# Kernel optimization log

Hardware: AMD Instinct MI355X
Metric: run time of the kernel (lower is better)

## Reference

```python
import jax, jax.numpy as jnp
import numpy as np

BUF = 16  # max polygon vertex buffer (convex 9-gon clipped by 4 half-planes -> <= 13 verts)


def _shoelace(V, c):
    # area of polygon stored in buffer V[:c]
    i = jnp.arange(V.shape[0])
    nxt = jnp.where(i + 1 < c, i + 1, 0)
    Vn = V[nxt]
    contrib = jnp.where(i < c, V[:, 0] * Vn[:, 1] - Vn[:, 0] * V[:, 1], 0.0)
    return 0.5 * jnp.abs(contrib.sum())


def _convex_hull(P):
    # exact convex hull of n small points; returns CCW-ordered vertex buffer [BUF,2] and count
    n = P.shape[0]
    d = P[None, :, :] - P[:, None, :]  # p_j - p_i
    minc = jnp.full((n, n), jnp.inf, P.dtype)
    for k in range(n):  # fixed small loop, keeps memory at [n,n]
        w = (P[k] - P)[:, None, :]
        minc = jnp.minimum(minc, d[..., 0] * w[..., 1] - d[..., 1] * w[..., 0])
    minc = jax.lax.stop_gradient(minc)  # hull membership is discrete
    edge = (minc >= -1e-6) & (~jnp.eye(n, dtype=bool))  # (i,j) is CCW hull edge iff all pts left
    hull = edge.any(1)
    cnt = hull.sum()
    cen = (P * hull[:, None]).sum(0) / jnp.maximum(cnt, 1)
    ang = jnp.arctan2(P[:, 1] - cen[1], P[:, 0] - cen[0])
    keyv = jnp.where(hull, jax.lax.stop_gradient(ang), jnp.inf)
    order = jnp.argsort(keyv)
    V = jnp.zeros((BUF, 2), P.dtype).at[:n].set(P[order])
    return V, cnt


def _clip(V, c, a, b):
    # Sutherland-Hodgman clip of convex polygon (V,c) by half-plane left of a->b
    i = jnp.arange(BUF)
    active = i < c
    nxt = jnp.where(i + 1 < c, i + 1, 0)
    nx = V[nxt]
    e = b - a
    s_cur = e[0] * (V[:, 1] - a[1]) - e[1] * (V[:, 0] - a[0])
    s_nxt = e[0] * (nx[:, 1] - a[1]) - e[1] * (nx[:, 0] - a[0])
    in_cur = s_cur >= 0
    in_nxt = s_nxt >= 0
    den = s_cur - s_nxt
    safe = jnp.abs(den) > 1e-9
    t = jnp.where(safe, s_cur / jnp.where(safe, den, 1.0), 0.0)
    ipt = V + t[:, None] * (nx - V)
    f_int = active & (in_cur != in_nxt)
    f_nxt = active & in_nxt
    pts = jnp.stack([ipt, nx], 1).reshape(2 * BUF, 2)
    flg = jnp.stack([f_int, f_nxt], 1).reshape(2 * BUF)
    pos = jnp.cumsum(flg) - 1
    idx = jnp.where(flg, pos, BUF)  # invalid slots dropped
    out = jnp.zeros((BUF, 2), V.dtype).at[idx].set(pts, mode='drop')
    return out, flg.sum()


def _order_ccw(Q):
    cen = Q.mean(0)
    ang = jnp.arctan2(Q[:, 1] - cen[1], Q[:, 0] - cen[0])
    return Q[jnp.argsort(jax.lax.stop_gradient(ang))]


def _per_point(gt4, p9):
    # giou_loss + out_of_box loss for one (gt quad, 9 pred points) pair
    gt = _order_ccw(gt4)
    Vp, cp = _convex_hull(p9)          # predicted convex polygon (OrientedRepPoints convex hull)
    a_pred = _shoelace(Vp, cp)
    a_gt = _shoelace(jnp.zeros((BUF, 2), gt.dtype).at[:4].set(gt), 4)
    V, c = Vp, cp
    for e in range(4):
        V, c = _clip(V, c, gt[e], gt[(e + 1) % 4])
    a_int = _shoelace(V, c)
    union = a_pred + a_gt - a_int
    iou = a_int / (union + 1e-16)
    Vh, ch = _convex_hull(jnp.concatenate([gt4, p9], 0))  # hull of all 13 points
    a_hull = _shoelace(Vh, ch)
    giou = iou - (a_hull - union) / (a_hull + 1e-16)
    # out-of-box distance: positive distance of pred points outside the gt quad edges
    b = jnp.roll(gt, -1, 0)
    e2 = b - gt
    rel = p9[:, None, :] - gt[None, :, :]
    s = (e2[None, :, 0] * rel[..., 1] - e2[None, :, 1] * rel[..., 0]) / (jnp.linalg.norm(e2, axis=1)[None, :] + 1e-9)
    oob = jax.nn.relu((-s).max(1)).mean()
    return 1.0 - giou, oob


def _assign(points_xy, points_lvl, gt_obb):
    # OBBPointAssigner: sequential per-GT closest-point assignment (pos_num=1, scale=4)
    xs = gt_obb[:, 0::2]
    ys = gt_obb[:, 1::2]
    xmin, xmax = xs.min(1), xs.max(1)
    ymin, ymax = ys.min(1), ys.max(1)
    cxy = jnp.stack([(xmin + xmax) / 2, (ymin + ymax) / 2], 1)
    wh = jnp.maximum(jnp.stack([xmax - xmin, ymax - ymin], 1), 1e-6)
    lvl_min, lvl_max = points_lvl.min(), points_lvl.max()
    glvl = jnp.clip(((jnp.log2(wh[:, 0] / 4.0) + jnp.log2(wh[:, 1] / 4.0)) / 2).astype(jnp.int32), lvl_min, lvl_max)
    K = gt_obb.shape[0]
    Np = points_xy.shape[0]

    def body(carry, g):
        inds, dist = carry
        c_xy, c_wh, c_lvl, gi = g
        dmask = points_lvl == c_lvl
        dd = jnp.linalg.norm((points_xy - c_xy) / c_wh, axis=1)
        dd = jnp.where(dmask, dd, jnp.inf)
        j = jnp.argmin(dd)
        md = dd[j]
        better = md < dist[j]
        inds = inds.at[j].set(jnp.where(better, gi + 1, inds[j]))
        dist = dist.at[j].set(jnp.where(better, md, dist[j]))
        return (inds, dist), None

    init = (jnp.zeros(Np, jnp.int32), jnp.full(Np, jnp.inf, points_xy.dtype))
    (inds, _), _ = jax.lax.scan(body, init, (cxy, wh, glvl, jnp.arange(K, dtype=jnp.int32)))
    return inds


def _stage(rep, inds, labels, gt_obb):
    posm = (labels > 0).astype(rep.dtype)
    gidx = jnp.maximum(inds - 1, 0)
    gt4 = gt_obb[gidx].reshape(-1, 4, 2)
    p9 = rep.reshape(-1, 9, 2)
    gl, oob = jax.vmap(_per_point)(gt4, p9)
    npos = jnp.maximum(posm.sum(), 1.0)
    return (gl * posm).sum() / npos, (oob * posm).sum() / npos


def _forward(rpi, rpr, cls, stride, gob, glab):
    stride = jax.lax.stop_gradient(stride)
    plvl = jnp.log2(stride).astype(jnp.int32)
    inds_i = _assign(jax.lax.stop_gradient(rpi[:, 8:10]), plvl, jax.lax.stop_gradient(gob))
    inds_r = _assign(jax.lax.stop_gradient(rpr[:, 8:10]), plvl, jax.lax.stop_gradient(gob))
    lab_i = jnp.where(inds_i > 0, glab[jnp.maximum(inds_i - 1, 0)], 0)
    lab_r = jnp.where(inds_r > 0, glab[jnp.maximum(inds_r - 1, 0)], 0)
    loc_i, sc_i = _stage(rpi, inds_i, lab_i, gob)
    loc_r, sc_r = _stage(rpr, inds_r, lab_r, gob)
    logp = jax.nn.log_softmax(cls, -1)
    cls_loss = -jnp.take_along_axis(logp, lab_r[:, None], 1).mean()
    return 1.0 * cls_loss + 0.3 * loc_i + 1.0 * loc_r + 0.05 * sc_i + 0.1 * sc_r


def setup_inputs() -> dict:
    key = jax.random.key(0)
    ks = jax.random.split(key, 8)
    strides = [8, 16, 32, 64, 128]
    batch = 2
    centers_list, stride_list = [], []
    for s in strides:
        hw = 1536 // s
        c = (jnp.arange(hw, dtype=jnp.float32) + 0.5) * s
        gx, gy = jnp.meshgrid(c, c, indexing='ij')
        cen = jnp.stack([gx.reshape(-1), gy.reshape(-1)], 1)
        cen = jnp.tile(cen, (batch, 1))
        centers_list.append(cen)
        stride_list.append(jnp.full((cen.shape[0],), float(s), jnp.float32))
    centers = jnp.concatenate(centers_list, 0)
    points_stride = jnp.concatenate(stride_list, 0)
    N = centers.shape[0]  # 98208
    base = jnp.tile(centers[:, None, :], (1, 9, 1)).reshape(N, 18)
    scale18 = jnp.repeat(points_stride[:, None], 18, 1)
    rpi = base + jax.random.normal(ks[0], (N, 18), jnp.float32) * scale18 * 1.5
    rpr = base + jax.random.normal(ks[1], (N, 18), jnp.float32) * scale18 * 1.0
    classification = jax.random.normal(ks[2], (N, 16), jnp.float32)
    K = 64
    cx = jax.random.uniform(ks[3], (K,), minval=128.0, maxval=1408.0)
    cy = jax.random.uniform(ks[4], (K,), minval=128.0, maxval=1408.0)
    w = jax.random.uniform(ks[5], (K,), minval=48.0, maxval=400.0)
    h = jax.random.uniform(ks[6], (K,), minval=48.0, maxval=400.0)
    th = jax.random.uniform(ks[7], (K,), minval=0.0, maxval=float(np.pi))
    ct, st = jnp.cos(th), jnp.sin(th)
    dx = jnp.stack([-w, w, w, -w], 1) / 2
    dy = jnp.stack([-h, -h, h, h], 1) / 2
    xs = cx[:, None] + dx * ct[:, None] - dy * st[:, None]
    ys = cy[:, None] + dx * st[:, None] + dy * ct[:, None]
    gt_obboxes = jnp.stack([xs, ys], 2).reshape(K, 8)
    gt_labels = jax.random.randint(jax.random.fold_in(key, 7), (K,), 1, 16)
    return {"rep_points_init": rpi, "rep_points_refine": rpr, "classification": classification,
            "points_stride": points_stride, "gt_obboxes": gt_obboxes, "gt_labels": gt_labels}


def reference(rep_points_init, rep_points_refine, classification, points_stride, gt_obboxes, gt_labels):
    return _forward(rep_points_init, rep_points_refine, classification, points_stride, gt_obboxes, gt_labels)
```

## Files before the change

kernel.cpp:

```cpp
#include <hip/hip_runtime.h>
#include <math.h>
#include <stdint.h>

#pragma clang fp contract(off)

#define SUB 16

struct WS {
  double sums[8];
  unsigned long long packed[128];
  int lo[8], hi[8];
  float gcx[64], gcy[64], gw[64], gh[64];
  int glvl[64];
  unsigned cntpub[2];
  unsigned done2;
  unsigned pad0;
  double clsPart[1024];
};

__global__ void __launch_bounds__(256) k_pre(const float* __restrict__ rpi,
                                             const float* __restrict__ rpr,
                                             const float* __restrict__ cls,
                                             const float* __restrict__ stridev,
                                             const float* __restrict__ gob,
                                             int N, int K, WS* ws) {
  __shared__ double sd[256];
  __shared__ int bnd[9];
  __shared__ int slmin, slmax;
  int t = threadIdx.x;
  float2* xyi = (float2*)(ws + 1);
  float2* xyr = xyi + N;

  if (blockIdx.x == 0) {
    if (t < 8) ws->sums[t] = 0.0;
    if (t < 128) ws->packed[t] = ~0ULL;
    if (t == 0) { ws->done2 = 0u; ws->cntpub[0] = 0u; ws->cntpub[1] = 0u; }
    if (t < 9) {
      float v = (float)(1 << t);
      int lo = 0, hi = N;
      while (lo < hi) { int mid = (lo + hi) >> 1; if (stridev[mid] < v) lo = mid + 1; else hi = mid; }
      bnd[t] = lo;
    }
    __syncthreads();
    if (t == 0) {
      int a = 7, b = 0;
      for (int l = 0; l < 8; l++) {
        int lo2 = bnd[l], hi2 = bnd[l + 1];
        ws->lo[l] = lo2; ws->hi[l] = hi2;
        if (hi2 > lo2) { if (l < a) a = l; if (l > b) b = l; }
      }
      slmin = a; slmax = b;
    }
    __syncthreads();
    if (t < K && t < 64) {
      const float* g = gob + t * 8;
      float x0 = g[0], x1 = g[2], x2 = g[4], x3 = g[6];
      float y0 = g[1], y1 = g[3], y2 = g[5], y3 = g[7];
      float xmin = fminf(fminf(x0, x1), fminf(x2, x3));
      float xmax = fmaxf(fmaxf(x0, x1), fmaxf(x2, x3));
      float ymin = fminf(fminf(y0, y1), fminf(y2, y3));
      float ymax = fmaxf(fmaxf(y0, y1), fmaxf(y2, y3));
      float w = fmaxf(xmax - xmin, 1e-6f);
      float h = fmaxf(ymax - ymin, 1e-6f);
      ws->gcx[t] = (xmin + xmax) * 0.5f;
      ws->gcy[t] = (ymin + ymax) * 0.5f;
      ws->gw[t] = w; ws->gh[t] = h;
      int gl = (int)((log2f(w * 0.25f) + log2f(h * 0.25f)) * 0.5f);
      gl = gl < slmin ? slmin : (gl > slmax ? slmax : gl);
      ws->glvl[t] = gl;
    }
  }

  double acc = 0.0;
  for (int i = blockIdx.x * 256 + t; i < N; i += gridDim.x * 256) {
    const float* pi = rpi + (size_t)i * 18;
    const float* pr = rpr + (size_t)i * 18;
    xyi[i] = *(const float2*)(pi + 8);
    xyr[i] = *(const float2*)(pr + 8);
    const float4* r = (const float4*)(cls + (size_t)i * 16);
    float4 q0 = r[0], q1 = r[1], q2 = r[2], q3 = r[3];
    float x[16] = {q0.x, q0.y, q0.z, q0.w, q1.x, q1.y, q1.z, q1.w,
                   q2.x, q2.y, q2.z, q2.w, q3.x, q3.y, q3.z, q3.w};
    float m = x[0];
    for (int j = 1; j < 16; j++) m = fmaxf(m, x[j]);
    float ssum = 0.f;
    for (int j = 0; j < 16; j++) ssum += expf(x[j] - m);
    acc += (double)(logf(ssum) + m - x[0]);
  }
  sd[t] = acc;
  __syncthreads();
  for (int off = 128; off > 0; off >>= 1) {
    if (t < off) sd[t] += sd[t + off];
    __syncthreads();
  }
  if (t == 0) ws->clsPart[blockIdx.x] = sd[0];
}

__global__ void __launch_bounds__(256) k_main(int N, int K, WS* ws) {
  __shared__ unsigned long long sb[256];
  int t = threadIdx.x;
  int b = blockIdx.x;
  int s = b % SUB;
  int ak = b / SUB;
  int a = ak / K;
  int k = ak % K;
  int L = ws->glvl[k];
  int lo = ws->lo[L], hi = ws->hi[L];
  float cx = ws->gcx[k], cy = ws->gcy[k], w = ws->gw[k], h = ws->gh[k];
  const float2* xy = (const float2*)(ws + 1) + (a ? N : 0);
  unsigned long long best = ~0ULL;
  for (int i = lo + s * 256 + t; i < hi; i += SUB * 256) {
    float2 p = xy[i];
    float dx = (p.x - cx) / w, dy = (p.y - cy) / h;
    float dd = sqrtf(dx * dx + dy * dy);
    unsigned long long pk = ((unsigned long long)__float_as_uint(dd) << 32) | (unsigned)i;
    if (pk < best) best = pk;
  }
  sb[t] = best;
  __syncthreads();
  for (int off = 128; off > 0; off >>= 1) {
    if (t < off) { unsigned long long o = sb[t + off]; if (o < sb[t]) sb[t] = o; }
    __syncthreads();
  }
  if (t == 0 && sb[0] != ~0ULL) atomicMin(&ws->packed[a * 64 + k], sb[0]);
}


__device__ __forceinline__ float shoe(const float* VX, const float* VY, int c) {
  float s = 0.f;
  #pragma unroll
  for (int i = 0; i < 16; i++) {
    if (i < c) {
      int nx = (i + 1 < c) ? ((i + 1 < 16) ? i + 1 : 15) : 0;
      s += VX[i] * VY[nx] - VX[nx] * VY[i];
    }
  }
  return 0.5f * fabsf(s);
}

__device__ __forceinline__ int clip_edge(const float* SX, const float* SY, float* DX, float* DY,
                                         int c, float ax, float ay, float bx, float by, int lane) {
  if (lane < 16) { DX[lane] = 0.f; DY[lane] = 0.f; }
  bool f_int = false, f_nxt = false;
  float ix = 0.f, iy = 0.f, nxv = 0.f, nyv = 0.f;
  if (lane < 16 && lane < c) {
    int nxt = (lane + 1 < c) ? lane + 1 : 0;
    if (nxt > 15) nxt = 15;
    float cxv = SX[lane], cyv = SY[lane];
    nxv = SX[nxt]; nyv = SY[nxt];
    float ex = bx - ax, ey = by - ay;
    float s_cur = ex * (cyv - ay) - ey * (cxv - ax);
    float s_nxt = ex * (nyv - ay) - ey * (nxv - ax);
    bool in_cur = s_cur >= 0.f, in_nxt = s_nxt >= 0.f;
    float den = s_cur - s_nxt;
    bool safe = fabsf(den) > 1e-9f;
    float tt = safe ? s_cur / den : 0.f;
    ix = cxv + tt * (nxv - cxv);
    iy = cyv + tt * (nyv - cyv);
    f_int = (in_cur != in_nxt);
    f_nxt = in_nxt;
  }
  unsigned long long bi = __ballot(f_int), bn = __ballot(f_nxt);
  unsigned long long lt = (1ULL << lane) - 1ULL;
  int below = __popcll(bi & lt) + __popcll(bn & lt);
  if (f_int && below < 16) { DX[below] = ix; DY[below] = iy; }
  int posn = below + (f_int ? 1 : 0);
  if (f_nxt && posn < 16) { DX[posn] = nxv; DY[posn] = nyv; }
  __syncthreads();
  return __popcll(bi) + __popcll(bn);
}

template <int NP>
__device__ __forceinline__ int hull_wave(const float* PX, const float* PY, int base,
                                         float* VX, float* VY, float* KEY, int lane) {
  constexpr int TOT = NP * NP;
  unsigned long long B0 = 0, B1 = 0, B2 = 0;
  {
    bool h = false;
    int idx = lane;
    if (idx < TOT) {
      int i = idx / NP, j = idx % NP;
      if (i != j) {
        float pix = PX[base + i], piy = PY[base + i];
        float dx = PX[base + j] - pix, dy = PY[base + j] - piy;
        float m = INFINITY;
        #pragma unroll
        for (int k = 0; k < NP; k++)
          m = fminf(m, dx * (PY[base + k] - piy) - dy * (PX[base + k] - pix));
        h = (m >= -1e-6f);
      }
    }
    B0 = __ballot(h);
  }
  if constexpr (TOT > 64) {
    bool h = false;
    int idx = lane + 64;
    if (idx < TOT) {
      int i = idx / NP, j = idx % NP;
      if (i != j) {
        float pix = PX[base + i], piy = PY[base + i];
        float dx = PX[base + j] - pix, dy = PY[base + j] - piy;
        float m = INFINITY;
        #pragma unroll
        for (int k = 0; k < NP; k++)
          m = fminf(m, dx * (PY[base + k] - piy) - dy * (PX[base + k] - pix));
        h = (m >= -1e-6f);
      }
    }
    B1 = __ballot(h);
  }
  if constexpr (TOT > 128) {
    bool h = false;
    int idx = lane + 128;
    if (idx < TOT) {
      int i = idx / NP, j = idx % NP;
      if (i != j) {
        float pix = PX[base + i], piy = PY[base + i];
        float dx = PX[base + j] - pix, dy = PY[base + j] - piy;
        float m = INFINITY;
        #pragma unroll
        for (int k = 0; k < NP; k++)
          m = fminf(m, dx * (PY[base + k] - piy) - dy * (PX[base + k] - pix));
        h = (m >= -1e-6f);
      }
    }
    B2 = __ballot(h);
  }
  bool hull_i = false;
  if (lane < NP) {
    int s = lane * NP, w = s >> 6, off = s & 63;
    unsigned long long Bw = (w == 0) ? B0 : ((w == 1) ? B1 : B2);
    unsigned long long Bw1 = (w == 0) ? B1 : ((w == 1) ? B2 : 0ULL);
    unsigned long long bits = Bw >> off;
    if (off) bits |= Bw1 << (64 - off);
    hull_i = (bits & ((1ULL << NP) - 1ULL)) != 0ULL;
  }
  unsigned long long hmask = __ballot(hull_i);
  int cnt = __popcll(hmask);
  float cx = 0.f, cy = 0.f;
  #pragma unroll
  for (int k = 0; k < NP; k++)
    if ((hmask >> k) & 1ULL) { cx += PX[base + k]; cy += PY[base + k]; }
  float dn = (float)(cnt > 1 ? cnt : 1);
  cx /= dn; cy /= dn;
  if (lane < NP)
    KEY[lane] = hull_i ? atan2f(PY[base + lane] - cy, PX[base + lane] - cx) : INFINITY;
  if (lane < 16) { VX[lane] = 0.f; VY[lane] = 0.f; }
  __syncthreads();
  if (lane < NP) {
    float ki = KEY[lane];
    int r = 0;
    #pragma unroll
    for (int j2 = 0; j2 < NP; j2++) {
      float kj = KEY[j2];
      r += (int)((kj < ki) || (kj == ki && j2 < lane));
    }
    VX[r] = PX[base + lane];
    VY[r] = PY[base + lane];
  }
  __syncthreads();
  return cnt;
}

__global__ void __launch_bounds__(64) k_post(const float* __restrict__ rpi,
                                             const float* __restrict__ rpr,
                                             const float* __restrict__ gob,
                                             const int* __restrict__ glab,
                                             const float* __restrict__ cls,
                                             int N, int nbCls, float* out, WS* ws) {
  __shared__ float PXs[16], PYs[16], VX[16], VY[16], DX[16], DY[16], KEY[16], RED[9];
  __shared__ int SJ[64];
  __shared__ unsigned long long SMK[64];
  __shared__ double SRED[64];
  __shared__ int islast;
  int lane = threadIdx.x;
  int b = blockIdx.x;
  int a = b >> 6, p = b & 63;

  unsigned long long pk = ws->packed[a * 64 + lane];
  bool valid = (pk != ~0ULL);
  SJ[lane] = valid ? (int)(unsigned)(pk & 0xffffffffu) : (-1 - lane);
  SMK[lane] = (pk & 0xffffffff00000000ULL) | (unsigned)lane;
  __syncthreads();
  bool win = false;
  if (valid) {
    int j = SJ[lane];
    unsigned long long me = SMK[lane];
    win = true;
    for (int o = 0; o < 64; o++)
      if (SJ[o] == j && SMK[o] < me) win = false;
  }
  unsigned long long wmask = __ballot(win);
  int cnt = __popcll(wmask);
  if (p == 0 && lane == 0) atomicExch(&ws->cntpub[a], (unsigned)cnt);

  bool active = (p < cnt);
  if (active) {
    int kk = 0;
    { int c2 = 0;
      for (int o = 0; o < 64; o++)
        if ((wmask >> o) & 1ULL) { if (c2 == p) { kk = o; break; } c2++; } }
    int j = SJ[kk];
    const float* rep = (a ? rpr : rpi) + (size_t)j * 18;
    const float* gt8 = gob + (size_t)kk * 8;
    if (lane < 4) { PXs[lane] = gt8[2 * lane]; PYs[lane] = gt8[2 * lane + 1]; }
    else if (lane < 13) { int q = lane - 4; PXs[lane] = rep[2 * q]; PYs[lane] = rep[2 * q + 1]; }
    __syncthreads();

    float cenx = (((PXs[0] + PXs[1]) + PXs[2]) + PXs[3]) / 4.f;
    float ceny = (((PYs[0] + PYs[1]) + PYs[2]) + PYs[3]) / 4.f;
    float angv[4];
    int r4[4];
    #pragma unroll
    for (int i = 0; i < 4; i++) angv[i] = atan2f(PYs[i] - ceny, PXs[i] - cenx);
    #pragma unroll
    for (int i = 0; i < 4; i++) {
      int r = 0;
      #pragma unroll
      for (int j2 = 0; j2 < 4; j2++)
        r += (int)((angv[j2] < angv[i]) || (angv[j2] == angv[i] && j2 < i));
      r4[i] = r;
    }
    float qx[4], qy[4];
    #pragma unroll
    for (int d = 0; d < 4; d++) {
      float sx = 0.f, sy = 0.f;
      #pragma unroll
      for (int i = 0; i < 4; i++) if (r4[i] == d) { sx = PXs[i]; sy = PYs[i]; }
      qx[d] = sx; qy[d] = sy;
    }

    int cp = hull_wave<9>(PXs, PYs, 4, VX, VY, KEY, lane);
    float a_pred = shoe(VX, VY, cp);

    float sgt = 0.f;
    #pragma unroll
    for (int i = 0; i < 4; i++) {
      int nx = (i + 1) & 3;
      sgt += qx[i] * qy[nx] - qx[nx] * qy[i];
    }
    float a_gt = 0.5f * fabsf(sgt);

    int c = cp;
    c = clip_edge(VX, VY, DX, DY, c, qx[0], qy[0], qx[1], qy[1], lane);
    c = clip_edge(DX, DY, VX, VY, c, qx[1], qy[1], qx[2], qy[2], lane);
    c = clip_edge(VX, VY, DX, DY, c, qx[2], qy[2], qx[3], qy[3], lane);
    c = clip_edge(DX, DY, VX, VY, c, qx[3], qy[3], qx[0], qy[0], lane);
    float a_int = shoe(VX, VY, c);

    float uni = a_pred + a_gt - a_int;
    float iou = a_int / (uni + 1e-16f);

    int ch = hull_wave<13>(PXs, PYs, 0, VX, VY, KEY, lane);
    float a_hull = shoe(VX, VY, ch);
    float giou = iou - (a_hull - uni) / (a_hull + 1e-16f);
    float gl = 1.f - giou;

    float mxv = -INFINITY;
    if (lane < 36) {
      int pp = lane >> 2, e = lane & 3;
      float ax = e == 0 ? qx[0] : e == 1 ? qx[1] : e == 2 ? qx[2] : qx[3];
      float ay = e == 0 ? qy[0] : e == 1 ? qy[1] : e == 2 ? qy[2] : qy[3];
      float bx2 = e == 0 ? qx[1] : e == 1 ? qx[2] : e == 2 ? qx[3] : qx[0];
      float by2 = e == 0 ? qy[1] : e == 1 ? qy[2] : e == 2 ? qy[3] : qy[0];
      float ex = bx2 - ax, ey = by2 - ay;
      float nrm = sqrtf(ex * ex + ey * ey) + 1e-9f;
      float px = PXs[4 + pp], py = PYs[4 + pp];
      float s = (ex * (py - ay) - ey * (px - ax)) / nrm;
      mxv = -s;
    }
    float o1 = __shfl_xor(mxv, 1); mxv = fmaxf(mxv, o1);
    float o2 = __shfl_xor(mxv, 2); mxv = fmaxf(mxv, o2);
    if (lane < 36 && (lane & 3) == 0) RED[lane >> 2] = fmaxf(mxv, 0.f);
    __syncthreads();
    if (lane == 0) {
      float acc = 0.f;
      #pragma unroll
      for (int pp = 0; pp < 9; pp++) acc += RED[pp];
      float oob = acc / 9.f;
      atomicAdd(&ws->sums[1 + a * 2], (double)gl);
      atomicAdd(&ws->sums[2 + a * 2], (double)oob);
      if (a == 1) {
        int lab = glab[kk];
        double corr = (double)cls[(size_t)j * 16] - (double)cls[(size_t)j * 16 + lab];
        atomicAdd(&ws->sums[0], corr);
      }
    }
  }

  __syncthreads();
  if (lane == 0) {
    __threadfence();
    unsigned d = atomicAdd(&ws->done2, 1u);
    islast = (d == gridDim.x - 1) ? 1 : 0;
  }
  __syncthreads();
  if (islast) {
    __threadfence();
    double sc = 0.0;
    for (int j = lane; j < nbCls; j += 64) sc += ws->clsPart[j];
    SRED[lane] = sc;
    __syncthreads();
    if (lane == 0) {
      double scls = 0.0;
      for (int j = 0; j < 64; j++) scls += SRED[j];
      double s0 = atomicAdd(&ws->sums[0], 0.0) + scls;
      double s1 = atomicAdd(&ws->sums[1], 0.0);
      double s2 = atomicAdd(&ws->sums[2], 0.0);
      double s3 = atomicAdd(&ws->sums[3], 0.0);
      double s4 = atomicAdd(&ws->sums[4], 0.0);
      unsigned c0 = atomicAdd(&ws->cntpub[0], 0u);
      unsigned c1 = atomicAdd(&ws->cntpub[1], 0u);
      double n0 = (double)(c0 > 1u ? c0 : 1u);
      double n1 = (double)(c1 > 1u ? c1 : 1u);
      out[0] = (float)(s0 / (double)N + 0.3 * (s1 / n0) + 1.0 * (s3 / n1) +
                       0.05 * (s2 / n0) + 0.1 * (s4 / n1));
    }
  }
}

extern "C" void kernel_launch(void* const* d_in, const int* in_sizes, int n_in,
                              void* d_out, int out_size, void* d_ws, size_t ws_size,
                              hipStream_t stream) {
  const float* rpi = (const float*)d_in[0];
  const float* rpr = (const float*)d_in[1];
  const float* cls = (const float*)d_in[2];
  const float* pstride = (const float*)d_in[3];
  const float* gob = (const float*)d_in[4];
  const int* glab = (const int*)d_in[5];
  int N = in_sizes[3];
  int K = in_sizes[5];
  if (K > 64) K = 64;
  WS* ws = (WS*)d_ws;

  int AB = 2 * K * SUB;
  int nb = (N + 255) / 256;
  if (nb > 1024) nb = 1024;
  if (nb < 1) nb = 1;
  k_pre<<<nb, 256, 0, stream>>>(rpi, rpr, cls, pstride, gob, N, K, ws);
  k_main<<<AB, 256, 0, stream>>>(N, K, ws);
  k_post<<<128, 64, 0, stream>>>(rpi, rpr, gob, glab, cls, N, nb, (float*)d_out, ws);
}
```

Baseline: 107.5 us.

## Fuse preprocessing and nearest-point search into one kernel with per-block slots

Merges the preprocessing kernel and the per-(gt,subset) nearest-point search into one grid-stride kernel. Each block now computes GT box parameters locally and derives levels from stride exponents. It does a warp-shuffle argmin per GT for points at the matching level and writes per-block minima to workspace slots instead of using global atomics. The post kernel then reduces those slots over all blocks. This removes one launch and the intermediate xy buffer, but adds a K-length loop of shuffle reductions per tile and a serial slot scan in the post kernel.

New measurement: 142.8 us. 1.33x slower.

```diff
diff --git a/kernel.cpp b/kernel.cpp
--- a/kernel.cpp
+++ b/kernel.cpp
@@ -4,125 +4,153 @@
 
 #pragma clang fp contract(off)
 
-#define SUB 16
-
 struct WS {
   double sums[8];
-  unsigned long long packed[128];
-  int lo[8], hi[8];
-  float gcx[64], gcy[64], gw[64], gh[64];
-  int glvl[64];
   unsigned cntpub[2];
   unsigned done2;
   unsigned pad0;
   double clsPart[1024];
 };
 
-__global__ void __launch_bounds__(256) k_pre(const float* __restrict__ rpi,
-                                             const float* __restrict__ rpr,
-                                             const float* __restrict__ cls,
-                                             const float* __restrict__ stridev,
-                                             const float* __restrict__ gob,
-                                             int N, int K, WS* ws) {
+__device__ __forceinline__ int lvl_of(float s) {
+  return (int)(__float_as_uint(s) >> 23) - 127;
+}
+
+__global__ void __launch_bounds__(256) k_fused(const float* __restrict__ rpi,
+                                               const float* __restrict__ rpr,
+                                               const float* __restrict__ cls,
+                                               const float* __restrict__ stridev,
+                                               const float* __restrict__ gob,
+                                               int N, int K, int nb, WS* ws) {
+  __shared__ float gcx[64], gcy[64], gw[64], gh[64];
+  __shared__ int glvlS[64];
+  __shared__ int sA[2];
+  __shared__ int LMIN[4], LMAX[4];
+  __shared__ unsigned long long wm0[4][64], wm1[4][64];
   __shared__ double sd[256];
-  __shared__ int bnd[9];
-  __shared__ int slmin, slmax;
   int t = threadIdx.x;
-  float2* xyi = (float2*)(ws + 1);
-  float2* xyr = xyi + N;
-
-  if (blockIdx.x == 0) {
+  int b = blockIdx.x;
+  int w = t >> 6, lane = t & 63;
+  unsigned long long* slots = (unsigned long long*)(ws + 1);
+
+  if (b == 0) {
     if (t < 8) ws->sums[t] = 0.0;
-    if (t < 128) ws->packed[t] = ~0ULL;
-    if (t == 0) { ws->done2 = 0u; ws->cntpub[0] = 0u; ws->cntpub[1] = 0u; }
-    if (t < 9) {
-      float v = (float)(1 << t);
-      int lo = 0, hi = N;
-      while (lo < hi) { int mid = (lo + hi) >> 1; if (stridev[mid] < v) lo = mid + 1; else hi = mid; }
-      bnd[t] = lo;
-    }
-    __syncthreads();
-    if (t == 0) {
-      int a = 7, b = 0;
-      for (int l = 0; l < 8; l++) {
-        int lo2 = bnd[l], hi2 = bnd[l + 1];
-        ws->lo[l] = lo2; ws->hi[l] = hi2;
-        if (hi2 > lo2) { if (l < a) a = l; if (l > b) b = l; }
-      }
-      slmin = a; slmax = b;
-    }
-    __syncthreads();
-    if (t < K && t < 64) {
-      const float* g = gob + t * 8;
-      float x0 = g[0], x1 = g[2], x2 = g[4], x3 = g[6];
-      float y0 = g[1], y1 = g[3], y2 = g[5], y3 = g[7];
-      float xmin = fminf(fminf(x0, x1), fminf(x2, x3));
-      float xmax = fmaxf(fmaxf(x0, x1), fmaxf(x2, x3));
-      float ymin = fminf(fminf(y0, y1), fminf(y2, y3));
-      float ymax = fmaxf(fmaxf(y0, y1), fmaxf(y2, y3));
-      float w = fmaxf(xmax - xmin, 1e-6f);
-      float h = fmaxf(ymax - ymin, 1e-6f);
-      ws->gcx[t] = (xmin + xmax) * 0.5f;
-      ws->gcy[t] = (ymin + ymax) * 0.5f;
-      ws->gw[t] = w; ws->gh[t] = h;
-      int gl = (int)((log2f(w * 0.25f) + log2f(h * 0.25f)) * 0.5f);
-      gl = gl < slmin ? slmin : (gl > slmax ? slmax : gl);
-      ws->glvl[t] = gl;
-    }
-  }
+    if (t == 0) ws->done2 = 0u;
+  }
+
+  wm0[w][lane] = ~0ULL;
+  wm1[w][lane] = ~0ULL;
+  if (t == 0) { sA[0] = lvl_of(stridev[0]); sA[1] = lvl_of(stridev[N - 1]); }
+
+  float pcx = 0.f, pcy = 0.f, pw = 1.f, ph = 1.f;
+  if (t < K) {
+    const float* g = gob + t * 8;
+    float x0 = g[0], x1 = g[2], x2 = g[4], x3 = g[6];
+    float y0 = g[1], y1 = g[3], y2 = g[5], y3 = g[7];
+    float xmin = fminf(fminf(x0, x1), fminf(x2, x3));
+    float xmax = fmaxf(fmaxf(x0, x1), fmaxf(x2, x3));
+    float ymin = fminf(fminf(y0, y1), fminf(y2, y3));
+    float ymax = fmaxf(fmaxf(y0, y1), fmaxf(y2, y3));
+    pw = fmaxf(xmax - xmin, 1e-6f);
+    ph = fmaxf(ymax - ymin, 1e-6f);
+    pcx = (xmin + xmax) * 0.5f;
+    pcy = (ymin + ymax) * 0.5f;
+  }
+  __syncthreads();
+  if (t < K) {
+    gcx[t] = pcx; gcy[t] = pcy; gw[t] = pw; gh[t] = ph;
+    int gl = (int)((log2f(pw * 0.25f) + log2f(ph * 0.25f)) * 0.5f);
+    int lmn = sA[0], lmx = sA[1];
+    gl = gl < lmn ? lmn : (gl > lmx ? lmx : gl);
+    glvlS[t] = gl;
+  }
+  __syncthreads();
 
   double acc = 0.0;
-  for (int i = blockIdx.x * 256 + t; i < N; i += gridDim.x * 256) {
-    const float* pi = rpi + (size_t)i * 18;
-    const float* pr = rpr + (size_t)i * 18;
-    xyi[i] = *(const float2*)(pi + 8);
-    xyr[i] = *(const float2*)(pr + 8);
-    const float4* r = (const float4*)(cls + (size_t)i * 16);
-    float4 q0 = r[0], q1 = r[1], q2 = r[2], q3 = r[3];
-    float x[16] = {q0.x, q0.y, q0.z, q0.w, q1.x, q1.y, q1.z, q1.w,
-                   q2.x, q2.y, q2.z, q2.w, q3.x, q3.y, q3.z, q3.w};
-    float m = x[0];
-    for (int j = 1; j < 16; j++) m = fmaxf(m, x[j]);
-    float ssum = 0.f;
-    for (int j = 0; j < 16; j++) ssum += expf(x[j] - m);
-    acc += (double)(logf(ssum) + m - x[0]);
-  }
+  for (int base = b * 256; base < N; base += nb * 256) {
+    int i = base + t;
+    bool valid = i < N;
+    int li = -1;
+    float xi = 0.f, yi = 0.f, xr = 0.f, yr = 0.f;
+    if (valid) {
+      li = lvl_of(stridev[i]);
+      float2 a2 = *(const float2*)(rpi + (size_t)i * 18 + 8);
+      xi = a2.x; yi = a2.y;
+      float2 b2 = *(const float2*)(rpr + (size_t)i * 18 + 8);
+      xr = b2.x; yr = b2.y;
+    }
+    int mn = valid ? li : 0x7fff;
+    int mx = valid ? li : -1;
+    #pragma unroll
+    for (int s = 1; s < 64; s <<= 1) {
+      int o = __shfl_xor(mn, s); mn = o < mn ? o : mn;
+      o = __shfl_xor(mx, s); mx = o > mx ? o : mx;
+    }
+    if (lane == 0) { LMIN[w] = mn; LMAX[w] = mx; }
+    __syncthreads();
+    int lmin = LMIN[0], lmax = LMAX[0];
+    #pragma unroll
+    for (int q = 1; q < 4; q++) {
+      lmin = LMIN[q] < lmin ? LMIN[q] : lmin;
+      lmax = LMAX[q] > lmax ? LMAX[q] : lmax;
+    }
+
+    for (int k = 0; k < K; k++) {
+      int gl = glvlS[k];
+      if (gl < lmin || gl > lmax) continue;
+      unsigned long long c0 = ~0ULL, c1 = ~0ULL;
+      if (valid && li == gl) {
+        float ccx = gcx[k], ccy = gcy[k], cw = gw[k], chh = gh[k];
+        float dx = (xi - ccx) / cw, dy = (yi - ccy) / chh;
+        float dd = sqrtf(dx * dx + dy * dy);
+        c0 = ((unsigned long long)__float_as_uint(dd) << 32) | (unsigned)i;
+        dx = (xr - ccx) / cw; dy = (yr - ccy) / chh;
+        dd = sqrtf(dx * dx + dy * dy);
+        c1 = ((unsigned long long)__float_as_uint(dd) << 32) | (unsigned)i;
+      }
+      #pragma unroll
+      for (int s = 1; s < 64; s <<= 1) {
+        unsigned long long o = __shfl_xor(c0, s); if (o < c0) c0 = o;
+        o = __shfl_xor(c1, s); if (o < c1) c1 = o;
+      }
+      if (lane == 0) {
+        if (c0 < wm0[w][k]) wm0[w][k] = c0;
+        if (c1 < wm1[w][k]) wm1[w][k] = c1;
+      }
+    }
+
+    if (valid) {
+      const float4* r = (const float4*)(cls + (size_t)i * 16);
+      float4 q0 = r[0], q1 = r[1], q2 = r[2], q3 = r[3];
+      float x[16] = {q0.x, q0.y, q0.z, q0.w, q1.x, q1.y, q1.z, q1.w,
+                     q2.x, q2.y, q2.z, q2.w, q3.x, q3.y, q3.z, q3.w};
+      float m = x[0];
+      for (int j = 1; j < 16; j++) m = fmaxf(m, x[j]);
+      float ssum = 0.f;
+      for (int j = 0; j < 16; j++) ssum += expf(x[j] - m);
+      acc += (double)(logf(ssum) + m - x[0]);
+    }
+    __syncthreads();
+  }
+
   sd[t] = acc;
   __syncthreads();
   for (int off = 128; off > 0; off >>= 1) {
     if (t < off) sd[t] += sd[t + off];
     __syncthreads();
   }
-  if (t == 0) ws->clsPart[blockIdx.x] = sd[0];
-}
-
-__global__ void __launch_bounds__(256) k_main(int N, int K, WS* ws) {
-  __shared__ unsigned long long sb[256];
-  int t = threadIdx.x;
-  int b = blockIdx.x;
-  int s = b % SUB;
-  int ak = b / SUB;
-  int a = ak / K;
-  int k = ak % K;
-  int L = ws->glvl[k];
-  int lo = ws->lo[L], hi = ws->hi[L];
-  float cx = ws->gcx[k], cy = ws->gcy[k], w = ws->gw[k], h = ws->gh[k];
-  const float2* xy = (const float2*)(ws + 1) + (a ? N : 0);
-  unsigned long long best = ~0ULL;
-  for (int i = lo + s * 256 + t; i < hi; i += SUB * 256) {
-    float2 p = xy[i];
-    float dx = (p.x - cx) / w, dy = (p.y - cy) / h;
-    float dd = sqrtf(dx * dx + dy * dy);
-    unsigned long long pk = ((unsigned long long)__float_as_uint(dd) << 32) | (unsigned)i;
-    if (pk < best) best = pk;
-  }
-  sb[t] = best;
-  __syncthreads();
-  for (int off = 128; off > 0; off >>= 1) {
-    if (t < off) { unsigned long long o = sb[t + off]; if (o < sb[t]) sb[t] = o; }
-    __syncthreads();
-  }
-  if (t == 0 && sb[0] != ~0ULL) atomicMin(&ws->packed[a * 64 + k], sb[0]);
+  if (t == 0) ws->clsPart[b] = sd[0];
+
+  if (t < 64) {
+    unsigned long long m0 = wm0[0][t], m1 = wm1[0][t];
+    #pragma unroll
+    for (int q = 1; q < 4; q++) {
+      if (wm0[q][t] < m0) m0 = wm0[q][t];
+      if (wm1[q][t] < m1) m1 = wm1[q][t];
+    }
+    slots[((size_t)b * 2 + 0) * 64 + t] = m0;
+    slots[((size_t)b * 2 + 1) * 64 + t] = m1;
+  }
 }
 
 
@@ -267,7 +295,7 @@
                                              const float* __restrict__ gob,
                                              const int* __restrict__ glab,
                                              const float* __restrict__ cls,
-                                             int N, int nbCls, float* out, WS* ws) {
+                                             int N, int nb, float* out, WS* ws) {
   __shared__ float PXs[16], PYs[16], VX[16], VY[16], DX[16], DY[16], KEY[16], RED[9];
   __shared__ int SJ[64];
   __shared__ unsigned long long SMK[64];
@@ -276,8 +304,19 @@
   int lane = threadIdx.x;
   int b = blockIdx.x;
   int a = b >> 6, p = b & 63;
-
-  unsigned long long pk = ws->packed[a * 64 + lane];
+  const unsigned long long* slots = (const unsigned long long*)(ws + 1);
+
+  unsigned long long pk = ~0ULL;
+  {
+    size_t stp = 128;
+    const unsigned long long* sp = slots + (size_t)a * 64 + lane;
+    #pragma unroll 8
+    for (int bb = 0; bb < nb; bb++) {
+      unsigned long long v = sp[(size_t)bb * stp];
+      if (v < pk) pk = v;
+    }
+  }
+
   bool valid = (pk != ~0ULL);
   SJ[lane] = valid ? (int)(unsigned)(pk & 0xffffffffu) : (-1 - lane);
   SMK[lane] = (pk & 0xffffffff00000000ULL) | (unsigned)lane;
@@ -398,7 +437,7 @@
   if (islast) {
     __threadfence();
     double sc = 0.0;
-    for (int j = lane; j < nbCls; j += 64) sc += ws->clsPart[j];
+    for (int j = lane; j < nb; j += 64) sc += ws->clsPart[j];
     SRED[lane] = sc;
     __syncthreads();
     if (lane == 0) {
@@ -433,11 +472,9 @@
   if (K > 64) K = 64;
   WS* ws = (WS*)d_ws;
 
-  int AB = 2 * K * SUB;
   int nb = (N + 255) / 256;
   if (nb > 1024) nb = 1024;
   if (nb < 1) nb = 1;
-  k_pre<<<nb, 256, 0, stream>>>(rpi, rpr, cls, pstride, gob, N, K, ws);
-  k_main<<<AB, 256, 0, stream>>>(N, K, ws);
+  k_fused<<<nb, 256, 0, stream>>>(rpi, rpr, cls, pstride, gob, N, K, nb, ws);
   k_post<<<128, 64, 0, stream>>>(rpi, rpr, gob, glab, cls, N, nb, (float*)d_out, ws);
 }
```
